# Optimization experiments

Measured on AMD Instinct MI355X. Metric: run time of the kernel, lower is better.

Reference implementation:

```python
import jax, jax.numpy as jnp
import numpy as np

BS, C_IN, NY, NX = 8, 256, 80, 80
C, NC, NA, N = 256, 80, 1, 16384
K = 3  # 3x3 sparse convs, padding 1


def setup_inputs() -> dict:
    key = jax.random.key(0)
    ks = jax.random.split(key, 16)
    w = lambda k, shape: jax.random.normal(k, shape, jnp.float32) * 0.02
    x = jax.random.normal(ks[0], (BS, C_IN, NY, NX), jnp.float32)
    bi = jax.random.randint(ks[1], (N,), 0, BS)
    yi = jax.random.randint(ks[2], (N,), 0, NY)
    xi = jax.random.randint(ks[3], (N,), 0, NX)
    indices = jnp.stack([bi, yi, xi], axis=1).astype(jnp.int64)
    return {
        'x': x,
        'indices': indices,
        'stem_w': w(ks[4], (C, C_IN)),        'stem_b': w(ks[5], (C,)),
        'cls_conv_w': w(ks[6], (C, C * K * K)), 'cls_conv_b': w(ks[7], (C,)),
        'reg_conv_w': w(ks[8], (C, C * K * K)), 'reg_conv_b': w(ks[9], (C,)),
        'cls_pred_w': w(ks[10], (NA * NC, C)),  'cls_pred_b': w(ks[11], (NA * NC,)),
        'reg_pred_w': w(ks[12], (NA * 4, C)),   'reg_pred_b': w(ks[13], (NA * 4,)),
        'obj_pred_w': w(ks[14], (NA * 1, C)),   'obj_pred_b': w(ks[15], (NA * 1,)),
    }


def _gather_patches(stem, indices):
    """Gather flattened KxK patches at (b,y,x) indices.

    Matches F.unfold ordering: flattened as [c, kh, kw].
    stem: [bs, c, ny, nx] -> returns [N, c*K*K].
    """
    pad = K // 2
    # NHWC padded feature map: [bs, ny+2p, nx+2p, c]
    padded = jnp.pad(stem.transpose(0, 2, 3, 1),
                     ((0, 0), (pad, pad), (pad, pad), (0, 0)))
    bi, yi, xi = indices[:, 0], indices[:, 1], indices[:, 2]
    d = jnp.arange(K)
    yy = yi[:, None, None] + d[None, :, None]   # [N, K, 1]
    xx = xi[:, None, None] + d[None, None, :]   # [N, 1, K]
    patches = padded[bi[:, None, None], yy, xx]  # [N, K, K, c]
    n = patches.shape[0]
    return patches.transpose(0, 3, 1, 2).reshape(n, -1)  # [N, c*K*K]


def reference(x, indices, stem_w, stem_b, cls_conv_w, cls_conv_b,
              reg_conv_w, reg_conv_b, cls_pred_w, cls_pred_b,
              reg_pred_w, reg_pred_b, obj_pred_w, obj_pred_b):
    # dense 1x1 stem conv + SiLU
    stem = jax.nn.silu(jnp.einsum('bchw,oc->bohw', x, stem_w)
                       + stem_b[None, :, None, None])
    # sparse 3x3 convs: gather patches -> linear -> SiLU
    pf = _gather_patches(stem, indices)                 # [N, C*9]
    cls_feat = jax.nn.silu(pf @ cls_conv_w.T + cls_conv_b)
    reg_feat = jax.nn.silu(pf @ reg_conv_w.T + reg_conv_b)
    n = pf.shape[0]
    cls = (cls_feat @ cls_pred_w.T + cls_pred_b).reshape(n, NA, NC)
    reg = (reg_feat @ reg_pred_w.T + reg_pred_b).reshape(n, NA, 4)
    obj = (reg_feat @ obj_pred_w.T + obj_pred_b).reshape(n, NA, 1)
    y_sp = jnp.concatenate([reg, obj, cls], axis=-1).reshape(n, NA * (5 + NC))
    return y_sp
```

## Files before the change

kernel.cpp:

```cpp
#include <hip/hip_runtime.h>

typedef unsigned short u16;
typedef __attribute__((ext_vector_type(4))) float f32x4;
typedef __attribute__((ext_vector_type(8))) short s16x8;

__device__ inline float bf2f(u16 u) {
    unsigned v = ((unsigned)u) << 16;
    return __builtin_bit_cast(float, v);
}
__device__ inline u16 f2bf(float f) {
    unsigned u = __builtin_bit_cast(unsigned, f);
    unsigned r = (u + 0x7FFFu + ((u >> 16) & 1u)) >> 16;
    return (u16)r;
}

typedef const __attribute__((address_space(1))) void* gptr_t;
typedef __attribute__((address_space(3))) void* lptr_t;
__device__ inline void gload16(const u16* gp, u16* lp) {
    __builtin_amdgcn_global_load_lds((gptr_t)gp, (lptr_t)lp, 16, 0, 0);
}

__global__ __launch_bounds__(256) void wsb_prep(const float* __restrict__ stem_w,
                                                u16* __restrict__ Wsb) {
    int base = blockIdx.x * 1024;
#pragma unroll
    for (int it = 0; it < 4; ++it) {
        int i = base + it * 256 + threadIdx.x;
        Wsb[i] = f2bf(stem_w[i]);
    }
}

__global__ __launch_bounds__(256, 4) void stem_prep(
    const float* __restrict__ x, const int* __restrict__ idx,
    const u16* __restrict__ Wsb, const float* __restrict__ stem_b,
    const float* __restrict__ cls_conv_w, const float* __restrict__ cls_conv_b,
    const float* __restrict__ reg_conv_w, const float* __restrict__ reg_conv_b,
    const float* __restrict__ cls_pred_w, const float* __restrict__ cls_pred_b,
    const float* __restrict__ reg_pred_w, const float* __restrict__ reg_pred_b,
    const float* __restrict__ obj_pred_w, const float* __restrict__ obj_pred_b,
    u16* __restrict__ stem, u16* __restrict__ Wc, u16* __restrict__ Wf,
    int* __restrict__ rowoff, float* __restrict__ bc, float* __restrict__ bp,
    u16* __restrict__ zpage) {
    __shared__ __align__(16) u16 lA[128 * 72];
    __shared__ __align__(16) u16 lB[64 * 64];
    const int blk = blockIdx.x;
    const int t = threadIdx.x;

    if (blk < 1600) {
        const int lane = t & 63;
        const int wid = t >> 6;
        const int wm = wid >> 1, wn = wid & 1;
        const int bx  = blk % 400;
        const int n0  = (blk / 400) * 64;
        const int b   = bx / 50;
        const int hwb = (bx % 50) * 128;

        const int srw = lane >> 3;
        const int cc  = lane & 7;
        const int gch = (cc ^ srw) * 8;
        const int arow = lane & 15;
        const int khi  = lane >> 4;
        const int sa   = arow & 7;

        const float* xb = x + (size_t)b * 256 * 6400 + hwb;
        const u16* Bp = Wsb + (size_t)(n0 + wid * 8 + srw) * 256 + gch;

        f32x4 acc[4][2] = {};

        for (int k0 = 0; k0 < 256; k0 += 64) {
#pragma unroll
            for (int r = 0; r < 2; ++r)
                gload16(Bp + (size_t)(r * 32) * 256 + k0,
                        lB + (r * 32 + wid * 8) * 64);
#pragma unroll
            for (int u = 0; u < 4; ++u) {
                const int hw  = (u & 1) * 64 + lane;
                const int oct = (u >> 1) * 4 + wid;
                union { u16 s[8]; s16x8 v; } pk;
#pragma unroll
                for (int jj = 0; jj < 8; ++jj)
                    pk.s[jj] = f2bf(xb[(size_t)(k0 + oct * 8 + jj) * 6400 + hw]);
                *(s16x8*)&lA[hw * 72 + oct * 8] = pk.v;
            }
            __syncthreads();
            s16x8 af[2][4], bfr[2][2];
#pragma unroll
            for (int f = 0; f < 4; ++f) {
                int ra = (wm * 64 + f * 16 + arow) * 72;
#pragma unroll
                for (int ks = 0; ks < 2; ++ks)
                    af[ks][f] = *(const s16x8*)&lA[ra + (ks * 4 + khi) * 8];
            }
#pragma unroll
            for (int jj = 0; jj < 2; ++jj) {
                int rb2 = (wn * 32 + jj * 16 + arow) * 64;
#pragma unroll
                for (int ks = 0; ks < 2; ++ks) {
                    int q = ks * 4 + khi;
                    bfr[ks][jj] = *(const s16x8*)&lB[rb2 + ((q ^ sa) << 3)];
                }
            }
#pragma unroll
            for (int ks = 0; ks < 2; ++ks)
#pragma unroll
                for (int i = 0; i < 4; ++i)
#pragma unroll
                    for (int jj = 0; jj < 2; ++jj)
                        acc[i][jj] = __builtin_amdgcn_mfma_f32_16x16x32_bf16(
                            af[ks][i], bfr[ks][jj], acc[i][jj], 0, 0, 0);
            __syncthreads();
        }

#pragma unroll
        for (int i = 0; i < 4; ++i) {
            int lr0 = wm * 64 + i * 16 + khi * 4;
#pragma unroll
            for (int jj = 0; jj < 2; ++jj) {
                int gc = n0 + wn * 32 + jj * 16 + arow;
                float bb = stem_b[gc];
#pragma unroll
                for (int r = 0; r < 4; ++r) {
                    float v = acc[i][jj][r] + bb;
                    v = v / (1.0f + __expf(-v));
                    stem[(size_t)(b * 6400 + hwb + lr0 + r) * 256 + gc] = f2bf(v);
                }
            }
        }
    } else if (blk < 2112) {
        int o = blk - 1600;
        const float* src = (o < 256) ? (cls_conv_w + (size_t)o * 2304)
                                     : (reg_conv_w + (size_t)(o - 256) * 2304);
        u16* dst = Wc + (size_t)o * 2304;
#pragma unroll
        for (int it = 0; it < 9; ++it) {
            int kk = it * 256 + t;
            int j = kk >> 8, c = kk & 255;
            dst[kk] = f2bf(src[c * 9 + j]);
        }
    } else if (blk < 2688) {
        int i = (blk - 2112) * 256 + t;
        int n = i / 9, j = i % 9;
        int b = idx[n * 3 + 0], y = idx[n * 3 + 1], xx0 = idx[n * 3 + 2];
        int yy = y + j / 3 - 1;
        int xx = xx0 + j % 3 - 1;
        rowoff[i] = ((unsigned)yy < 80u && (unsigned)xx < 80u)
                        ? (b * 6400 + yy * 80 + xx) * 256 : -1;
    } else if (blk < 2720) {
        int base = (blk - 2688) * 2048;
#pragma unroll
        for (int it = 0; it < 8; ++it) {
            int i = base + it * 256 + t;
            int o = i >> 9, k = i & 511;
            float v = 0.f;
            if (o < 4)       { if (k >= 256) v = reg_pred_w[o * 256 + (k - 256)]; }
            else if (o == 4) { if (k >= 256) v = obj_pred_w[k - 256]; }
            else if (o < 85) { if (k < 256)  v = cls_pred_w[(o - 5) * 256 + k]; }
            Wf[i] = f2bf(v);
        }
    } else {
        for (int i = t; i < 512; i += 256)
            bc[i] = (i < 256) ? cls_conv_b[i] : reg_conv_b[i - 256];
        if (t < 128) {
            float v = 0.f;
            if (t < 4) v = reg_pred_b[t];
            else if (t == 4) v = obj_pred_b[0];
            else if (t < 85) v = cls_pred_b[t - 5];
            bp[t] = v;
        }
        zpage[t] = 0;
    }
}

__global__ __launch_bounds__(256, 4) void gemm_conv(
    const u16* __restrict__ stem, const int* __restrict__ rowoff,
    const u16* __restrict__ zpage, const u16* __restrict__ B,
    const float* __restrict__ bias, u16* __restrict__ D) {
    __shared__ __align__(16) u16 lA[128 * 64];
    __shared__ __align__(16) u16 lB[64 * 64];
    const int tid = threadIdx.x;
    const int lane = tid & 63;
    const int wid = tid >> 6;
    const int wm = wid >> 1, wn = wid & 1;
    const int m0 = blockIdx.x * 128;
    const int n0 = blockIdx.y * 64;

    const int srw = lane >> 3;
    const int cc  = lane & 7;
    const int gch = (cc ^ srw) * 8;
    const int arow = lane & 15;
    const int khi  = lane >> 4;
    const int sa   = arow & 7;

    int ro[4][9];
#pragma unroll
    for (int r = 0; r < 4; ++r) {
        const int rb = (m0 + r * 32 + wid * 8 + srw) * 9;
#pragma unroll
        for (int j = 0; j < 9; ++j) ro[r][j] = rowoff[rb + j];
    }
    const u16* Bp = B + (size_t)(n0 + wid * 8 + srw) * 2304 + gch;

    f32x4 acc[4][2] = {};

#pragma unroll
    for (int j = 0; j < 9; ++j) {
#pragma unroll
        for (int q4 = 0; q4 < 4; ++q4) {
            const int c0 = q4 << 6;
            const int k0 = j * 256 + c0;
#pragma unroll
            for (int r = 0; r < 2; ++r)
                gload16(Bp + (size_t)(r * 32) * 2304 + k0,
                        lB + (r * 32 + wid * 8) * 64);
#pragma unroll
            for (int r = 0; r < 4; ++r) {
                int roff = ro[r][j];
                const u16* srcA = (roff < 0) ? (zpage + gch)
                                             : (stem + roff + c0 + gch);
                gload16(srcA, lA + (r * 32 + wid * 8) * 64);
            }
            __syncthreads();
            s16x8 af[2][4], bfr[2][2];
#pragma unroll
            for (int f = 0; f < 4; ++f) {
                int ra = (wm * 64 + f * 16 + arow) * 64;
#pragma unroll
                for (int ks = 0; ks < 2; ++ks) {
                    int q = ks * 4 + khi;
                    af[ks][f] = *(const s16x8*)&lA[ra + ((q ^ sa) << 3)];
                }
            }
#pragma unroll
            for (int jj = 0; jj < 2; ++jj) {
                int rb2 = (wn * 32 + jj * 16 + arow) * 64;
#pragma unroll
                for (int ks = 0; ks < 2; ++ks) {
                    int q = ks * 4 + khi;
                    bfr[ks][jj] = *(const s16x8*)&lB[rb2 + ((q ^ sa) << 3)];
                }
            }
#pragma unroll
            for (int ks = 0; ks < 2; ++ks)
#pragma unroll
                for (int i = 0; i < 4; ++i)
#pragma unroll
                    for (int jj = 0; jj < 2; ++jj)
                        acc[i][jj] = __builtin_amdgcn_mfma_f32_16x16x32_bf16(
                            af[ks][i], bfr[ks][jj], acc[i][jj], 0, 0, 0);
            __syncthreads();
        }
    }

#pragma unroll
    for (int i = 0; i < 4; ++i) {
        int gr0 = m0 + wm * 64 + i * 16 + khi * 4;
#pragma unroll
        for (int jj = 0; jj < 2; ++jj) {
            int gc = n0 + wn * 32 + jj * 16 + arow;
            float bb = bias[gc];
#pragma unroll
            for (int r = 0; r < 4; ++r) {
                float v = acc[i][jj][r] + bb;
                v = v / (1.0f + __expf(-v));
                D[(size_t)(gr0 + r) * 512 + gc] = f2bf(v);
            }
        }
    }
}

__global__ __launch_bounds__(256, 4) void gemm_pred(
    const u16* __restrict__ A, const u16* __restrict__ B,
    const float* __restrict__ bias, float* __restrict__ D) {
    __shared__ __align__(16) u16 lA[64 * 64];
    __shared__ __align__(16) u16 lB[64 * 64];
    const int tid = threadIdx.x;
    const int lane = tid & 63;
    const int wid = tid >> 6;
    const int wm = wid >> 1, wn = wid & 1;
    const int m0 = blockIdx.x * 64;
    const int n0 = blockIdx.y * 64;

    const int srw = lane >> 3;
    const int cc  = lane & 7;
    const int arow = lane & 15;
    const int khi  = lane >> 4;

    f32x4 acc[2][2] = {};

    for (int k0 = 0; k0 < 512; k0 += 64) {
        const int gch = (cc ^ srw) * 8;
#pragma unroll
        for (int r = 0; r < 2; ++r) {
            int row = r * 32 + wid * 8 + srw;
            gload16(A + (size_t)(m0 + row) * 512 + k0 + gch,
                    lA + (r * 32 + wid * 8) * 64);
            gload16(B + (size_t)(n0 + row) * 512 + k0 + gch,
                    lB + (r * 32 + wid * 8) * 64);
        }
        __syncthreads();
        s16x8 af[2][2], bfr[2][2];
        const int sa = arow & 7;
#pragma unroll
        for (int f = 0; f < 2; ++f) {
            int ra = (wm * 32 + f * 16 + arow) * 64;
            int rb = (wn * 32 + f * 16 + arow) * 64;
#pragma unroll
            for (int ks = 0; ks < 2; ++ks) {
                int q = ks * 4 + khi;
                af[ks][f]  = *(const s16x8*)&lA[ra + ((q ^ sa) << 3)];
                bfr[ks][f] = *(const s16x8*)&lB[rb + ((q ^ sa) << 3)];
            }
        }
#pragma unroll
        for (int ks = 0; ks < 2; ++ks)
#pragma unroll
            for (int i = 0; i < 2; ++i)
#pragma unroll
                for (int jj = 0; jj < 2; ++jj)
                    acc[i][jj] = __builtin_amdgcn_mfma_f32_16x16x32_bf16(
                        af[ks][i], bfr[ks][jj], acc[i][jj], 0, 0, 0);
        __syncthreads();
    }

#pragma unroll
    for (int i = 0; i < 2; ++i) {
        int gr0 = m0 + wm * 32 + i * 16 + khi * 4;
#pragma unroll
        for (int jj = 0; jj < 2; ++jj) {
            int gc = n0 + wn * 32 + jj * 16 + arow;
            if (gc >= 85) continue;
            float bb = bias[gc];
#pragma unroll
            for (int r = 0; r < 4; ++r)
                D[(size_t)(gr0 + r) * 85 + gc] = acc[i][jj][r] + bb;
        }
    }
}

extern "C" void kernel_launch(void* const* d_in, const int* in_sizes, int n_in,
                              void* d_out, int out_size, void* d_ws, size_t ws_size,
                              hipStream_t stream) {
    const float* x          = (const float*)d_in[0];
    const int*   idx        = (const int*)d_in[1];
    const float* stem_w     = (const float*)d_in[2];
    const float* stem_b     = (const float*)d_in[3];
    const float* cls_conv_w = (const float*)d_in[4];
    const float* cls_conv_b = (const float*)d_in[5];
    const float* reg_conv_w = (const float*)d_in[6];
    const float* reg_conv_b = (const float*)d_in[7];
    const float* cls_pred_w = (const float*)d_in[8];
    const float* cls_pred_b = (const float*)d_in[9];
    const float* reg_pred_w = (const float*)d_in[10];
    const float* reg_pred_b = (const float*)d_in[11];
    const float* obj_pred_w = (const float*)d_in[12];
    const float* obj_pred_b = (const float*)d_in[13];
    float* out = (float*)d_out;
    char* ws = (char*)d_ws;

    u16*  stem   = (u16*)(ws);
    u16*  feat   = (u16*)(ws + 26214400);
    u16*  Wc     = (u16*)(ws + 42991616);
    u16*  Wf     = (u16*)(ws + 45350912);
    u16*  Wsb    = (u16*)(ws + 45481984);
    int*  rowoff = (int*)(ws + 45613056);
    u16*  zpage  = (u16*)(ws + 46202880);
    float* bc    = (float*)(ws + 46203392);
    float* bp    = (float*)(ws + 46205440);

    wsb_prep<<<64, 256, 0, stream>>>(stem_w, Wsb);
    stem_prep<<<2721, 256, 0, stream>>>(x, idx, Wsb, stem_b,
                                        cls_conv_w, cls_conv_b, reg_conv_w, reg_conv_b,
                                        cls_pred_w, cls_pred_b, reg_pred_w, reg_pred_b,
                                        obj_pred_w, obj_pred_b,
                                        stem, Wc, Wf, rowoff, bc, bp, zpage);
    gemm_conv<<<dim3(128, 8), 256, 0, stream>>>(stem, rowoff, zpage, Wc, bc, feat);
    gemm_pred<<<dim3(256, 2), 256, 0, stream>>>(feat, Wf, bp, out);
}
```

Baseline: 93.53 us.

## Triple-buffer LDS tiles with K=32 stages to overlap loads and MFMA

Replaces the single-buffered 64-wide K loop, which issued loads, synchronized, computed and synchronized again, with a 3-stage ring of 32-wide K tiles. Loads for stage s+2 are issued while stage s is computed, using vmcnt waits and a single barrier per step. The intent is to hide global-to-LDS latency behind the MFMA work. In exchange there are twice as many pipeline steps, more barriers per unit of K, and the LDS swizzle is reworked to fit 32-element rows.

```diff
diff --git a/kernel.cpp b/kernel.cpp
--- a/kernel.cpp
+++ b/kernel.cpp
@@ -175,8 +175,8 @@
     const u16* __restrict__ stem, const int* __restrict__ rowoff,
     const u16* __restrict__ zpage, const u16* __restrict__ B,
     const float* __restrict__ bias, u16* __restrict__ D) {
-    __shared__ __align__(16) u16 lA[128 * 64];
-    __shared__ __align__(16) u16 lB[64 * 64];
+    __shared__ __align__(16) u16 lA[3][128 * 32];
+    __shared__ __align__(16) u16 lB[3][64 * 32];
     const int tid = threadIdx.x;
     const int lane = tid & 63;
     const int wid = tid >> 6;
@@ -184,72 +184,69 @@
     const int m0 = blockIdx.x * 128;
     const int n0 = blockIdx.y * 64;
 
-    const int srw = lane >> 3;
-    const int cc  = lane & 7;
-    const int gch = (cc ^ srw) * 8;
+    const int srw = lane >> 2;
+    const int cc  = lane & 3;
+    const int swz = (srw >> 1) & 3;
+    const int gch = (cc ^ swz) * 8;
     const int arow = lane & 15;
     const int khi  = lane >> 4;
-    const int sa   = arow & 7;
-
-    int ro[4][9];
-#pragma unroll
-    for (int r = 0; r < 4; ++r) {
-        const int rb = (m0 + r * 32 + wid * 8 + srw) * 9;
+    const int sa   = (arow >> 1) & 3;
+    const int rq   = (khi ^ sa) << 3;
+
+    int ro[2][9];
+#pragma unroll
+    for (int r = 0; r < 2; ++r) {
+        const int rb = (m0 + r * 64 + wid * 16 + srw) * 9;
 #pragma unroll
         for (int j = 0; j < 9; ++j) ro[r][j] = rowoff[rb + j];
     }
-    const u16* Bp = B + (size_t)(n0 + wid * 8 + srw) * 2304 + gch;
+    const u16* Bp = B + (size_t)(n0 + wid * 16 + srw) * 2304 + gch;
 
     f32x4 acc[4][2] = {};
 
-#pragma unroll
-    for (int j = 0; j < 9; ++j) {
-#pragma unroll
-        for (int q4 = 0; q4 < 4; ++q4) {
-            const int c0 = q4 << 6;
-            const int k0 = j * 256 + c0;
-#pragma unroll
-            for (int r = 0; r < 2; ++r)
-                gload16(Bp + (size_t)(r * 32) * 2304 + k0,
-                        lB + (r * 32 + wid * 8) * 64);
-#pragma unroll
-            for (int r = 0; r < 4; ++r) {
-                int roff = ro[r][j];
-                const u16* srcA = (roff < 0) ? (zpage + gch)
-                                             : (stem + roff + c0 + gch);
-                gload16(srcA, lA + (r * 32 + wid * 8) * 64);
-            }
-            __syncthreads();
-            s16x8 af[2][4], bfr[2][2];
-#pragma unroll
-            for (int f = 0; f < 4; ++f) {
-                int ra = (wm * 64 + f * 16 + arow) * 64;
-#pragma unroll
-                for (int ks = 0; ks < 2; ++ks) {
-                    int q = ks * 4 + khi;
-                    af[ks][f] = *(const s16x8*)&lA[ra + ((q ^ sa) << 3)];
-                }
-            }
-#pragma unroll
-            for (int jj = 0; jj < 2; ++jj) {
-                int rb2 = (wn * 32 + jj * 16 + arow) * 64;
-#pragma unroll
-                for (int ks = 0; ks < 2; ++ks) {
-                    int q = ks * 4 + khi;
-                    bfr[ks][jj] = *(const s16x8*)&lB[rb2 + ((q ^ sa) << 3)];
-                }
-            }
-#pragma unroll
-            for (int ks = 0; ks < 2; ++ks)
-#pragma unroll
-                for (int i = 0; i < 4; ++i)
-#pragma unroll
-                    for (int jj = 0; jj < 2; ++jj)
-                        acc[i][jj] = __builtin_amdgcn_mfma_f32_16x16x32_bf16(
-                            af[ks][i], bfr[ks][jj], acc[i][jj], 0, 0, 0);
-            __syncthreads();
-        }
-    }
+#define STAGE(TS, BI)                                                           \
+    {   const int c0_ = ((TS) & 7) << 5;                                        \
+        const int jt_ = (TS) >> 3;                                              \
+        _Pragma("unroll")                                                       \
+        for (int r = 0; r < 2; ++r) {                                           \
+            int roff_ = ro[r][jt_];                                             \
+            const u16* s_ = (roff_ < 0) ? (zpage + gch)                         \
+                                        : (stem + roff_ + c0_ + gch);           \
+            gload16(s_, &lA[BI][(r * 64 + wid * 16) * 32]);                     \
+        }                                                                       \
+        gload16(Bp + (TS) * 32, &lB[BI][(wid * 16) * 32]); }
+
+    STAGE(0, 0);
+    STAGE(1, 1);
+    asm volatile("s_waitcnt vmcnt(3)" ::: "memory");
+    __builtin_amdgcn_s_barrier();
+
+#pragma unroll
+    for (int s = 0; s < 72; ++s) {
+        if (s + 2 < 72) STAGE(s + 2, (s + 2) % 3);
+        const int bi = s % 3;
+        s16x8 af[4], bf[2];
+#pragma unroll
+        for (int f = 0; f < 4; ++f)
+            af[f] = *(const s16x8*)&lA[bi][(wm * 64 + f * 16 + arow) * 32 + rq];
+#pragma unroll
+        for (int jj = 0; jj < 2; ++jj)
+            bf[jj] = *(const s16x8*)&lB[bi][(wn * 32 + jj * 16 + arow) * 32 + rq];
+#pragma unroll
+        for (int i = 0; i < 4; ++i)
+#pragma unroll
+            for (int jj = 0; jj < 2; ++jj)
+                acc[i][jj] = __builtin_amdgcn_mfma_f32_16x16x32_bf16(
+                    af[i], bf[jj], acc[i][jj], 0, 0, 0);
+        if (s < 70) {
+            asm volatile("s_waitcnt vmcnt(3)" ::: "memory");
+            __builtin_amdgcn_s_barrier();
+        } else if (s == 70) {
+            asm volatile("s_waitcnt vmcnt(0)" ::: "memory");
+            __builtin_amdgcn_s_barrier();
+        }
+    }
+#undef STAGE
 
 #pragma unroll
     for (int i = 0; i < 4; ++i) {
```

After: 105.1 us. +12.3%, slower.
